# Kernel tuning notes

Hardware: AMD Instinct MI355X
Metric: run time of the kernel (lower is better)

## Reference

```python
import jax, jax.numpy as jnp
import numpy as np

N_NODES = 50000
N_EDGES = 1600000
D = 64  # in_dim = hidden_dim = out_dim
R = 8   # num_rels


def setup_inputs() -> dict:
    key = jax.random.key(0)
    ks = jax.random.split(key, 9)
    adj = jax.random.randint(ks[0], (2, N_EDGES), 0, N_NODES, dtype=jnp.int32)
    features = jax.random.normal(ks[1], (N_NODES, D), dtype=jnp.float32)
    edge_type = jax.random.randint(ks[2], (N_EDGES,), 0, R, dtype=jnp.int32)
    s = 1.0 / np.sqrt(D)
    W1 = jax.random.normal(ks[3], (R, D, D), dtype=jnp.float32) * s
    root1 = jax.random.normal(ks[4], (D, D), dtype=jnp.float32) * s
    b1 = jnp.zeros((D,), dtype=jnp.float32)
    W2 = jax.random.normal(ks[5], (R, D, D), dtype=jnp.float32) * s
    root2 = jax.random.normal(ks[6], (D, D), dtype=jnp.float32) * s
    b2 = jnp.zeros((D,), dtype=jnp.float32)
    return {"adj": adj, "features": features, "edge_type": edge_type,
            "W1": W1, "root1": root1, "b1": b1,
            "W2": W2, "root2": root2, "b2": b2}


def _rgcn_layer(x, edge_index, edge_type, W, root, bias):
    # FastRGCNConv, aggr='add': out_i = sum_{(j,r)->i} W_r x_j + root^T x_i + b
    src, dst = edge_index[0], edge_index[1]
    # pre-transform all nodes under every relation: [R, N, F]
    h = jnp.einsum('nd,rdf->rnf', x, W)
    msg = h[edge_type, src]                      # [E, F] gather per edge
    agg = jax.ops.segment_sum(msg, dst, num_segments=x.shape[0])
    return agg + x @ root + bias


def reference(adj, features, edge_type, W1, root1, b1, W2, root2, b2):
    x = _rgcn_layer(features, adj, edge_type, W1, root1, b1)
    x = jax.nn.relu(x)
    x = _rgcn_layer(x, adj, edge_type, W2, root2, b2)
    return x
```

## Files before the change

### kernel.cpp

```cpp
#include <hip/hip_runtime.h>
#include <cstdint>
#include <cstddef>

#define DF 64
#define NREL 8
#define DPB 64
#define DPB_SHIFT 6
#define NBMAX 1024
#define EPB 4096
#define BCAP 3072
#define NKEY 512

typedef __attribute__((ext_vector_type(8))) short bf16x8;
typedef __attribute__((ext_vector_type(4))) float f32x4;

static __device__ __forceinline__ unsigned short f2bf(float f) {
  unsigned int u = __float_as_uint(f);
  u += 0x7FFFu + ((u >> 16) & 1u);
  return (unsigned short)(u >> 16);
}
static __device__ __forceinline__ float bf2f(unsigned short s) {
  return __uint_as_float((unsigned int)s << 16);
}

__global__ __launch_bounds__(512) void prep(
    const float* __restrict__ W1, const float* __restrict__ rt1,
    const float* __restrict__ W2, const float* __restrict__ rt2,
    bf16x8* __restrict__ frag,
    const float* __restrict__ x, unsigned short* __restrict__ xb, int n8,
    int* __restrict__ bcnt, int NB)
{
  const int b = blockIdx.x;
  const int t = threadIdx.x;

  if (b < 18) {
    const float* W = (b < 8)  ? (W1 + (size_t)b * 4096)
                   : (b == 8) ? rt1
                   : (b < 17) ? (W2 + (size_t)(b - 9) * 4096)
                              : rt2;
    const int ft = t >> 7;
    const int ks = (t >> 6) & 1;
    const int l  = t & 63;
    const int col = ft * 16 + (l & 15);
    const int k0  = ks * 32 + (l >> 4) * 8;
    bf16x8 f;
#pragma unroll
    for (int j = 0; j < 8; ++j)
      f[j] = (short)f2bf(W[(size_t)(k0 + j) * 64 + col]);
    frag[(((size_t)b * 4 + ft) * 2 + ks) * 64 + l] = f;
    return;
  }

  if (b == 18) {
    for (int i = t; i < NB; i += 512) bcnt[i] = 0;
  }

  const int i = (b - 18) * 512 + t;
  if (i < n8) {
    const float4 v0 = *(const float4*)&x[(size_t)i * 8];
    const float4 v1 = *(const float4*)&x[(size_t)i * 8 + 4];
    uint4 pk;
    pk.x = (unsigned)f2bf(v0.x) | ((unsigned)f2bf(v0.y) << 16);
    pk.y = (unsigned)f2bf(v0.z) | ((unsigned)f2bf(v0.w) << 16);
    pk.z = (unsigned)f2bf(v1.x) | ((unsigned)f2bf(v1.y) << 16);
    pk.w = (unsigned)f2bf(v1.z) | ((unsigned)f2bf(v1.w) << 16);
    *(uint4*)&xb[(size_t)i * 8] = pk;
  }
}

__global__ __launch_bounds__(512) void bucket_count(
    const int* __restrict__ dst, int* __restrict__ bcnt,
    int* __restrict__ relof, int E, int NB)
{
  __shared__ int lh[NBMAX];
  const int t = threadIdx.x;
  for (int i = t; i < NB; i += 512) lh[i] = 0;
  __syncthreads();
  const int base = blockIdx.x * EPB;
  const int cnt = min(EPB, E - base);
  for (int k = t; k < cnt; k += 512)
    atomicAdd(&lh[dst[base + k] >> DPB_SHIFT], 1);
  __syncthreads();
  int* rrow = relof + (size_t)blockIdx.x * NB;
  for (int i = t; i < NB; i += 512) {
    int c = lh[i];
    rrow[i] = c ? atomicAdd(&bcnt[i], c) : 0;
  }
}

__global__ __launch_bounds__(1024) void scan_buckets(
    const int* __restrict__ bcnt, int* __restrict__ boff, int NB, int E)
{
  __shared__ int sc[1024];
  const int t = threadIdx.x;
  int v = (t < NB) ? bcnt[t] : 0;
  sc[t] = v;
  __syncthreads();
  for (int off = 1; off < 1024; off <<= 1) {
    int u = (t >= off) ? sc[t - off] : 0;
    __syncthreads();
    sc[t] += u;
    __syncthreads();
  }
  if (t < NB) boff[t] = sc[t] - v;
  if (t == 0) boff[NB] = E;
}

__global__ __launch_bounds__(512) void bin_scatter(
    const int* __restrict__ src, const int* __restrict__ dst,
    const int* __restrict__ et,
    const int* __restrict__ boff, const int* __restrict__ relof,
    unsigned int* __restrict__ binned, int E, int NB)
{
  __shared__ int cur[NBMAX];
  const int t = threadIdx.x;
  const int* rrow = relof + (size_t)blockIdx.x * NB;
  for (int i = t; i < NB; i += 512) cur[i] = boff[i] + rrow[i];
  __syncthreads();
  const int base = blockIdx.x * EPB;
  const int cnt = min(EPB, E - base);
  for (int k = t; k < cnt; k += 512) {
    int e = base + k;
    int d = dst[e];
    int pos = atomicAdd(&cur[d >> DPB_SHIFT], 1);
    binned[pos] = ((unsigned)et[e] << 24) | ((unsigned)src[e] << 7) |
                  ((unsigned)d & (DPB - 1));
  }
}

static __device__ __forceinline__ void gadd(
    float* __restrict__ acc, const uint4& u)
{
  acc[0] += bf2f((unsigned short)u.x);
  acc[1] += bf2f((unsigned short)(u.x >> 16));
  acc[2] += bf2f((unsigned short)u.y);
  acc[3] += bf2f((unsigned short)(u.y >> 16));
  acc[4] += bf2f((unsigned short)u.z);
  acc[5] += bf2f((unsigned short)(u.z >> 16));
  acc[6] += bf2f((unsigned short)u.w);
  acc[7] += bf2f((unsigned short)(u.w >> 16));
}

__global__ __launch_bounds__(512) void gather_sum(
    const unsigned int* __restrict__ binned,
    const int* __restrict__ boff,
    const unsigned short* __restrict__ xb,
    unsigned short* __restrict__ s,
    int N)
{
  __shared__ unsigned int srt[BCAP];
  __shared__ int h[NKEY], sc[NKEY], cur[NKEY];
  __shared__ int wsum[8];
  const int t = threadIdx.x;
  const int b = blockIdx.x;
  const int beg = boff[b], end = boff[b + 1];
  const int m = min(end - beg, BCAP);

  h[t] = 0;
  __syncthreads();
  for (int k = t; k < m; k += 512) {
    unsigned w = binned[beg + k];
    atomicAdd(&h[((w & (DPB - 1)) << 3) | (w >> 24)], 1);
  }
  __syncthreads();

  {
    const int lane = t & 63;
    const int wv = t >> 6;
    int v = h[t];
    int incl = v;
#pragma unroll
    for (int off = 1; off < 64; off <<= 1) {
      int u = __shfl_up(incl, off);
      if (lane >= off) incl += u;
    }
    if (lane == 63) wsum[wv] = incl;
    __syncthreads();
    int wo = 0;
    for (int w2 = 0; w2 < wv; ++w2) wo += wsum[w2];
    sc[t] = incl + wo;
    cur[t] = sc[t] - v;
  }
  __syncthreads();

  for (int k = t; k < m; k += 512) {
    unsigned w = binned[beg + k];
    int pos = atomicAdd(&cur[((w & (DPB - 1)) << 3) | (w >> 24)], 1);
    srt[pos] = w;
  }
  __syncthreads();

  const int nl = t >> 3;
  const int node = (b << DPB_SHIFT) + nl;
  const int l8 = (t & 7) * 8;
  if (node >= N) return;
  const int ovf = end - beg - BCAP;

#define XADDR(wv) ((const uint4*)&xb[(((size_t)(((wv) >> 7) & 0x1FFFFu)) << 6) + l8])
  for (int r = 0; r < NREL; ++r) {
    const int kk = (nl << 3) | r;
    int p = sc[kk] - h[kk];
    const int pe = sc[kk];
    float acc[8];
#pragma unroll
    for (int i = 0; i < 8; ++i) acc[i] = 0.f;

    for (; p + 3 < pe; p += 4) {
      unsigned w0 = srt[p],     w1 = srt[p + 1];
      unsigned w2 = srt[p + 2], w3 = srt[p + 3];
      uint4 u0 = *XADDR(w0), u1 = *XADDR(w1);
      uint4 u2 = *XADDR(w2), u3 = *XADDR(w3);
      gadd(acc, u0); gadd(acc, u1); gadd(acc, u2); gadd(acc, u3);
    }
    for (; p < pe; ++p) {
      unsigned w0 = srt[p];
      uint4 u0 = *XADDR(w0);
      gadd(acc, u0);
    }
    if (ovf > 0) {
      for (int k = 0; k < ovf; ++k) {
        unsigned w0 = binned[beg + BCAP + k];
        if ((int)(w0 & (DPB - 1)) == nl && (int)(w0 >> 24) == r) {
          uint4 u0 = *XADDR(w0);
          gadd(acc, u0);
        }
      }
    }

    uint4 pk;
    pk.x = (unsigned)f2bf(acc[0]) | ((unsigned)f2bf(acc[1]) << 16);
    pk.y = (unsigned)f2bf(acc[2]) | ((unsigned)f2bf(acc[3]) << 16);
    pk.z = (unsigned)f2bf(acc[4]) | ((unsigned)f2bf(acc[5]) << 16);
    pk.w = (unsigned)f2bf(acc[6]) | ((unsigned)f2bf(acc[7]) << 16);
    *(uint4*)&s[(((size_t)node * NREL + r) << 6) + l8] = pk;
  }
#undef XADDR
}

__global__ __launch_bounds__(256) void gemm_fused(
    const unsigned short* __restrict__ s,
    const unsigned short* __restrict__ xb,
    const bf16x8* __restrict__ wfrag,
    const float* __restrict__ bias,
    float* __restrict__ out,
    unsigned short* __restrict__ xbn,
    int N, int do_relu)
{
  const int tid = threadIdx.x;
  const int l  = tid & 63;
  const int w  = tid >> 6;
  const int n0 = blockIdx.x * 128 + w * 32;
  const int lr = l & 15;
  const int lg = l >> 4;

  f32x4 acc[4][2];
#pragma unroll
  for (int mt = 0; mt < 4; ++mt)
#pragma unroll
    for (int nt = 0; nt < 2; ++nt)
      acc[mt][nt] = (f32x4)(0.f);

  const int node0 = n0 + lr;
  const int node1 = n0 + 16 + lr;

  for (int r = 0; r < 9; ++r) {
    const bf16x8* wf = wfrag + (size_t)r * 512;
    bf16x8 a[4][2];
#pragma unroll
    for (int mt = 0; mt < 4; ++mt)
#pragma unroll
      for (int ks = 0; ks < 2; ++ks)
        a[mt][ks] = wf[(mt * 2 + ks) * 64 + l];

    bf16x8 b[2][2];
#pragma unroll
    for (int nt = 0; nt < 2; ++nt) {
      const int node = nt ? node1 : node0;
#pragma unroll
      for (int ks = 0; ks < 2; ++ks) {
        if (node < N) {
          const unsigned short* bp = (r < 8)
              ? &s[(((size_t)node * NREL + r) << 6) + ks * 32 + lg * 8]
              : &xb[((size_t)node << 6) + ks * 32 + lg * 8];
          b[nt][ks] = *(const bf16x8*)bp;
        } else {
          b[nt][ks] = (bf16x8)(short)0;
        }
      }
    }

#pragma unroll
    for (int ks = 0; ks < 2; ++ks)
#pragma unroll
      for (int mt = 0; mt < 4; ++mt)
#pragma unroll
        for (int nt = 0; nt < 2; ++nt)
          acc[mt][nt] = __builtin_amdgcn_mfma_f32_16x16x32_bf16(
              a[mt][ks], b[nt][ks], acc[mt][nt], 0, 0, 0);
  }

#pragma unroll
  for (int nt = 0; nt < 2; ++nt) {
    const int node = nt ? node1 : node0;
    if (node < N) {
#pragma unroll
      for (int mt = 0; mt < 4; ++mt) {
        const int f0 = mt * 16 + lg * 4;
        float4 bb = *(const float4*)&bias[f0];
        float4 v = make_float4(acc[mt][nt][0] + bb.x,
                               acc[mt][nt][1] + bb.y,
                               acc[mt][nt][2] + bb.z,
                               acc[mt][nt][3] + bb.w);
        if (do_relu) {
          v.x = fmaxf(v.x, 0.f); v.y = fmaxf(v.y, 0.f);
          v.z = fmaxf(v.z, 0.f); v.w = fmaxf(v.w, 0.f);
        }
        *(float4*)&out[((size_t)node << 6) + f0] = v;
        if (xbn) {
          uint2 pk;
          pk.x = (unsigned)f2bf(v.x) | ((unsigned)f2bf(v.y) << 16);
          pk.y = (unsigned)f2bf(v.z) | ((unsigned)f2bf(v.w) << 16);
          *(uint2*)&xbn[((size_t)node << 6) + f0] = pk;
        }
      }
    }
  }
}

__global__ __launch_bounds__(128) void rgcn_transform(
    const float* __restrict__ x,
    const float* __restrict__ Wc,
    unsigned short* __restrict__ hb,
    int N)
{
  const int r = blockIdx.y;
  const float* W = Wc + (size_t)r * DF * DF;

  __shared__ float Ws[DF * DF];
  __shared__ float Xs[128 * 65];

  const int tid = threadIdx.x;
  const int n0 = blockIdx.x * 128;
  const int nrem = N - n0;

  {
    const float4* Wv = (const float4*)W;
    float4* Wsv = (float4*)Ws;
#pragma unroll
    for (int j = 0; j < 8; ++j) Wsv[tid + j * 128] = Wv[tid + j * 128];
  }
#pragma unroll
  for (int j = 0; j < 16; ++j) {
    int idx = tid + j * 128;
    int n = idx >> 4;
    int c4 = (idx & 15) * 4;
    float4 v = make_float4(0.f, 0.f, 0.f, 0.f);
    if (n < nrem) v = *(const float4*)&x[(size_t)(n0 + n) * DF + c4];
    float* p = &Xs[n * 65 + c4];
    p[0] = v.x; p[1] = v.y; p[2] = v.z; p[3] = v.w;
  }
  __syncthreads();

  const int fg = (tid & 7) * 8;
  const int ng = (tid >> 3) * 8;

  float4 a0[8], a1[8];
#pragma unroll
  for (int i = 0; i < 8; ++i) {
    a0[i] = make_float4(0.f, 0.f, 0.f, 0.f);
    a1[i] = make_float4(0.f, 0.f, 0.f, 0.f);
  }

#pragma unroll 4
  for (int d = 0; d < DF; ++d) {
    float4 w0 = *(const float4*)&Ws[d * DF + fg];
    float4 w1 = *(const float4*)&Ws[d * DF + fg + 4];
#pragma unroll
    for (int i = 0; i < 8; ++i) {
      float xv = Xs[(ng + i) * 65 + d];
      a0[i].x += xv * w0.x; a0[i].y += xv * w0.y;
      a0[i].z += xv * w0.z; a0[i].w += xv * w0.w;
      a1[i].x += xv * w1.x; a1[i].y += xv * w1.y;
      a1[i].z += xv * w1.z; a1[i].w += xv * w1.w;
    }
  }

#pragma unroll
  for (int i = 0; i < 8; ++i) {
    int n = ng + i;
    if (n < nrem) {
      uint4 pk;
      pk.x = (unsigned)f2bf(a0[i].x) | ((unsigned)f2bf(a0[i].y) << 16);
      pk.y = (unsigned)f2bf(a0[i].z) | ((unsigned)f2bf(a0[i].w) << 16);
      pk.z = (unsigned)f2bf(a1[i].x) | ((unsigned)f2bf(a1[i].y) << 16);
      pk.w = (unsigned)f2bf(a1[i].z) | ((unsigned)f2bf(a1[i].w) << 16);
      unsigned short* op = hb + (((size_t)r * N + (n0 + n)) << 6) + fg;
      *(uint4*)op = pk;
    }
  }
}

__global__ __launch_bounds__(128) void rgcn_root_epilogue(
    const float* __restrict__ x,
    const float* __restrict__ root,
    const float* __restrict__ bias,
    float* __restrict__ out,
    int N, int mode)
{
  __shared__ float Ws[DF * DF];
  __shared__ float Xs[128 * 65];

  const int tid = threadIdx.x;
  const int n0 = blockIdx.x * 128;
  const int nrem = N - n0;

  {
    const float4* Wv = (const float4*)root;
    float4* Wsv = (float4*)Ws;
#pragma unroll
    for (int j = 0; j < 8; ++j) Wsv[tid + j * 128] = Wv[tid + j * 128];
  }
#pragma unroll
  for (int j = 0; j < 16; ++j) {
    int idx = tid + j * 128;
    int n = idx >> 4;
    int c4 = (idx & 15) * 4;
    float4 v = make_float4(0.f, 0.f, 0.f, 0.f);
    if (n < nrem) v = *(const float4*)&x[(size_t)(n0 + n) * DF + c4];
    float* p = &Xs[n * 65 + c4];
    p[0] = v.x; p[1] = v.y; p[2] = v.z; p[3] = v.w;
  }
  __syncthreads();

  const int fg = (tid & 7) * 8;
  const int ng = (tid >> 3) * 8;

  float4 a0[8], a1[8];
#pragma unroll
  for (int i = 0; i < 8; ++i) {
    a0[i] = make_float4(0.f, 0.f, 0.f, 0.f);
    a1[i] = make_float4(0.f, 0.f, 0.f, 0.f);
  }

#pragma unroll 4
  for (int d = 0; d < DF; ++d) {
    float4 w0 = *(const float4*)&Ws[d * DF + fg];
    float4 w1 = *(const float4*)&Ws[d * DF + fg + 4];
#pragma unroll
    for (int i = 0; i < 8; ++i) {
      float xv = Xs[(ng + i) * 65 + d];
      a0[i].x += xv * w0.x; a0[i].y += xv * w0.y;
      a0[i].z += xv * w0.z; a0[i].w += xv * w0.w;
      a1[i].x += xv * w1.x; a1[i].y += xv * w1.y;
      a1[i].z += xv * w1.z; a1[i].w += xv * w1.w;
    }
  }

  float4 bb0 = *(const float4*)&bias[fg];
  float4 bb1 = *(const float4*)&bias[fg + 4];

#pragma unroll
  for (int i = 0; i < 8; ++i) {
    int n = ng + i;
    if (n < nrem) {
      float* op = out + (size_t)(n0 + n) * DF + fg;
      float4 o0 = *(float4*)op;
      float4 o1 = *(float4*)(op + 4);
      o0.x += a0[i].x + bb0.x; o0.y += a0[i].y + bb0.y;
      o0.z += a0[i].z + bb0.z; o0.w += a0[i].w + bb0.w;
      o1.x += a1[i].x + bb1.x; o1.y += a1[i].y + bb1.y;
      o1.z += a1[i].z + bb1.z; o1.w += a1[i].w + bb1.w;
      if (mode == 1) {
        o0.x = fmaxf(o0.x, 0.f); o0.y = fmaxf(o0.y, 0.f);
        o0.z = fmaxf(o0.z, 0.f); o0.w = fmaxf(o0.w, 0.f);
        o1.x = fmaxf(o1.x, 0.f); o1.y = fmaxf(o1.y, 0.f);
        o1.z = fmaxf(o1.z, 0.f); o1.w = fmaxf(o1.w, 0.f);
      }
      *(float4*)op = o0;
      *(float4*)(op + 4) = o1;
    }
  }
}

__global__ __launch_bounds__(256) void rgcn_scatter(
    const int* __restrict__ src, const int* __restrict__ dst,
    const int* __restrict__ et,
    const unsigned short* __restrict__ hb,
    float* __restrict__ out,
    int E, int N, int r0, int r1)
{
  long long g = (long long)blockIdx.x * 256 + threadIdx.x;
  int e = (int)(g >> 4);
  if (e >= E) return;
  int r = et[e];
  if (r < r0 || r >= r1) return;
  int f4 = ((int)g & 15) * 4;
  int s = src[e];
  int d = dst[e];
  ushort4 u = *(const ushort4*)&hb[(((size_t)(r - r0) * N + s) << 6) + f4];
  float* o = out + ((size_t)d << 6) + f4;
  atomicAdd(o + 0, bf2f(u.x));
  atomicAdd(o + 1, bf2f(u.y));
  atomicAdd(o + 2, bf2f(u.z));
  atomicAdd(o + 3, bf2f(u.w));
}

extern "C" void kernel_launch(void* const* d_in, const int* in_sizes, int n_in,
                              void* d_out, int out_size, void* d_ws, size_t ws_size,
                              hipStream_t stream) {
  const int* adj    = (const int*)d_in[0];
  const float* feat = (const float*)d_in[1];
  const int* et     = (const int*)d_in[2];
  const float* W1   = (const float*)d_in[3];
  const float* rt1  = (const float*)d_in[4];
  const float* b1   = (const float*)d_in[5];
  const float* W2   = (const float*)d_in[6];
  const float* rt2  = (const float*)d_in[7];
  const float* b2   = (const float*)d_in[8];

  const int E = in_sizes[0] / 2;
  const int N = in_sizes[1] / DF;
  const int* srcp = adj;
  const int* dstp = adj + E;

  float* out = (float*)d_out;
  const size_t ND = (size_t)N * DF;
  const int nblk = (N + 127) / 128;
  const int NB = (N + DPB - 1) >> DPB_SHIFT;
  const int ebk = (E + EPB - 1) / EPB;

  const size_t wfrag_elems = (size_t)18 * 512;
  const size_t need = 8 * ND * 2 + ND * 2 + ND * 2 + wfrag_elems * 16 +
                      (size_t)E * 4 + (size_t)ebk * NB * 4 +
                      ((size_t)2 * NB + 1) * 4;

  if (ws_size >= need && NB <= NBMAX && N < (1 << 17)) {
    unsigned short* s   = (unsigned short*)d_ws;
    unsigned short* xb  = s + 8 * ND;
    unsigned short* xb2 = xb + ND;
    bf16x8* wfrag = (bf16x8*)(xb2 + ND);
    unsigned int* binned = (unsigned int*)(wfrag + wfrag_elems);
    int* relof = (int*)(binned + E);
    int* bcnt = relof + (size_t)ebk * NB;
    int* boff = bcnt + NB;

    const int n8 = (int)(ND / 8);
    prep<<<18 + (n8 + 511) / 512, 512, 0, stream>>>(
        W1, rt1, W2, rt2, wfrag, feat, xb, n8, bcnt, NB);

    bucket_count<<<ebk, 512, 0, stream>>>(dstp, bcnt, relof, E, NB);
    scan_buckets<<<1, 1024, 0, stream>>>(bcnt, boff, NB, E);
    bin_scatter<<<ebk, 512, 0, stream>>>(srcp, dstp, et, boff, relof,
                                         binned, E, NB);

    gather_sum<<<NB, 512, 0, stream>>>(binned, boff, xb, s, N);
    gemm_fused<<<nblk, 256, 0, stream>>>(s, xb, wfrag, b1, out, xb2, N, 1);

    gather_sum<<<NB, 512, 0, stream>>>(binned, boff, xb2, s, N);
    gemm_fused<<<nblk, 256, 0, stream>>>(s, xb2, wfrag + (size_t)9 * 512,
                                         b2, out, nullptr, N, 0);
    return;
  }

  size_t per_rel = ND * sizeof(unsigned short);
  size_t xmid_b = ND * sizeof(float);
  int RC = 1;
  if (ws_size > per_rel + xmid_b) {
    size_t rc = (ws_size - xmid_b) / per_rel;
    RC = rc >= NREL ? NREL : (int)rc;
  }
  unsigned short* hb = (unsigned short*)d_ws;
  float* xmid = (float*)((char*)d_ws + (size_t)RC * per_rel);
  const int sblk = (int)(((size_t)E * 16 + 255) / 256);

  for (int layer = 0; layer < 2; ++layer) {
    const float* xin = layer ? xmid : feat;
    const float* W   = layer ? W2 : W1;
    const float* rt  = layer ? rt2 : rt1;
    const float* bs  = layer ? b2 : b1;
    float* o         = layer ? out : xmid;

    hipMemsetAsync(o, 0, ND * sizeof(float), stream);
    for (int r0 = 0; r0 < NREL; r0 += RC) {
      int rc = (NREL - r0) < RC ? (NREL - r0) : RC;
      rgcn_transform<<<dim3(nblk, rc), 128, 0, stream>>>(
          xin, W + (size_t)r0 * DF * DF, hb, N);
      rgcn_scatter<<<sblk, 256, 0, stream>>>(
          srcp, dstp, et, hb, o, E, N, r0, r0 + rc);
    }
    rgcn_root_epilogue<<<nblk, 128, 0, stream>>>(xin, rt, bs, o, N,
                                                 layer == 0 ? 1 : 2);
  }
}
```

Measured before the change: 150.2 us.

## Fuse per-relation gather-sum with MFMA transform into one kernel per layer

```diff
diff --git a/kernel.cpp b/kernel.cpp
--- a/kernel.cpp
+++ b/kernel.cpp
@@ -10,6 +10,7 @@
 #define EPB 4096
 #define BCAP 3072
 #define NKEY 512
+#define SBST 72
 
 typedef __attribute__((ext_vector_type(8))) short bf16x8;
 typedef __attribute__((ext_vector_type(4))) float f32x4;
@@ -141,104 +142,9 @@
   acc[7] += bf2f((unsigned short)(u.w >> 16));
 }
 
-__global__ __launch_bounds__(512) void gather_sum(
+__global__ __launch_bounds__(512, 4) void gather_gemm(
     const unsigned int* __restrict__ binned,
     const int* __restrict__ boff,
-    const unsigned short* __restrict__ xb,
-    unsigned short* __restrict__ s,
-    int N)
-{
-  __shared__ unsigned int srt[BCAP];
-  __shared__ int h[NKEY], sc[NKEY], cur[NKEY];
-  __shared__ int wsum[8];
-  const int t = threadIdx.x;
-  const int b = blockIdx.x;
-  const int beg = boff[b], end = boff[b + 1];
-  const int m = min(end - beg, BCAP);
-
-  h[t] = 0;
-  __syncthreads();
-  for (int k = t; k < m; k += 512) {
-    unsigned w = binned[beg + k];
-    atomicAdd(&h[((w & (DPB - 1)) << 3) | (w >> 24)], 1);
-  }
-  __syncthreads();
-
-  {
-    const int lane = t & 63;
-    const int wv = t >> 6;
-    int v = h[t];
-    int incl = v;
-#pragma unroll
-    for (int off = 1; off < 64; off <<= 1) {
-      int u = __shfl_up(incl, off);
-      if (lane >= off) incl += u;
-    }
-    if (lane == 63) wsum[wv] = incl;
-    __syncthreads();
-    int wo = 0;
-    for (int w2 = 0; w2 < wv; ++w2) wo += wsum[w2];
-    sc[t] = incl + wo;
-    cur[t] = sc[t] - v;
-  }
-  __syncthreads();
-
-  for (int k = t; k < m; k += 512) {
-    unsigned w = binned[beg + k];
-    int pos = atomicAdd(&cur[((w & (DPB - 1)) << 3) | (w >> 24)], 1);
-    srt[pos] = w;
-  }
-  __syncthreads();
-
-  const int nl = t >> 3;
-  const int node = (b << DPB_SHIFT) + nl;
-  const int l8 = (t & 7) * 8;
-  if (node >= N) return;
-  const int ovf = end - beg - BCAP;
-
-#define XADDR(wv) ((const uint4*)&xb[(((size_t)(((wv) >> 7) & 0x1FFFFu)) << 6) + l8])
-  for (int r = 0; r < NREL; ++r) {
-    const int kk = (nl << 3) | r;
-    int p = sc[kk] - h[kk];
-    const int pe = sc[kk];
-    float acc[8];
-#pragma unroll
-    for (int i = 0; i < 8; ++i) acc[i] = 0.f;
-
-    for (; p + 3 < pe; p += 4) {
-      unsigned w0 = srt[p],     w1 = srt[p + 1];
-      unsigned w2 = srt[p + 2], w3 = srt[p + 3];
-      uint4 u0 = *XADDR(w0), u1 = *XADDR(w1);
-      uint4 u2 = *XADDR(w2), u3 = *XADDR(w3);
-      gadd(acc, u0); gadd(acc, u1); gadd(acc, u2); gadd(acc, u3);
-    }
-    for (; p < pe; ++p) {
-      unsigned w0 = srt[p];
-      uint4 u0 = *XADDR(w0);
-      gadd(acc, u0);
-    }
-    if (ovf > 0) {
-      for (int k = 0; k < ovf; ++k) {
-        unsigned w0 = binned[beg + BCAP + k];
-        if ((int)(w0 & (DPB - 1)) == nl && (int)(w0 >> 24) == r) {
-          uint4 u0 = *XADDR(w0);
-          gadd(acc, u0);
-        }
-      }
-    }
-
-    uint4 pk;
-    pk.x = (unsigned)f2bf(acc[0]) | ((unsigned)f2bf(acc[1]) << 16);
-    pk.y = (unsigned)f2bf(acc[2]) | ((unsigned)f2bf(acc[3]) << 16);
-    pk.z = (unsigned)f2bf(acc[4]) | ((unsigned)f2bf(acc[5]) << 16);
-    pk.w = (unsigned)f2bf(acc[6]) | ((unsigned)f2bf(acc[7]) << 16);
-    *(uint4*)&s[(((size_t)node * NREL + r) << 6) + l8] = pk;
-  }
-#undef XADDR
-}
-
-__global__ __launch_bounds__(256) void gemm_fused(
-    const unsigned short* __restrict__ s,
     const unsigned short* __restrict__ xb,
     const bf16x8* __restrict__ wfrag,
     const float* __restrict__ bias,
@@ -246,82 +152,164 @@
     unsigned short* __restrict__ xbn,
     int N, int do_relu)
 {
-  const int tid = threadIdx.x;
-  const int l  = tid & 63;
-  const int w  = tid >> 6;
-  const int n0 = blockIdx.x * 128 + w * 32;
-  const int lr = l & 15;
-  const int lg = l >> 4;
-
-  f32x4 acc[4][2];
-#pragma unroll
-  for (int mt = 0; mt < 4; ++mt)
-#pragma unroll
-    for (int nt = 0; nt < 2; ++nt)
-      acc[mt][nt] = (f32x4)(0.f);
-
-  const int node0 = n0 + lr;
-  const int node1 = n0 + 16 + lr;
-
-  for (int r = 0; r < 9; ++r) {
-    const bf16x8* wf = wfrag + (size_t)r * 512;
-    bf16x8 a[4][2];
-#pragma unroll
-    for (int mt = 0; mt < 4; ++mt)
-#pragma unroll
-      for (int ks = 0; ks < 2; ++ks)
-        a[mt][ks] = wf[(mt * 2 + ks) * 64 + l];
-
-    bf16x8 b[2][2];
-#pragma unroll
-    for (int nt = 0; nt < 2; ++nt) {
-      const int node = nt ? node1 : node0;
-#pragma unroll
-      for (int ks = 0; ks < 2; ++ks) {
-        if (node < N) {
-          const unsigned short* bp = (r < 8)
-              ? &s[(((size_t)node * NREL + r) << 6) + ks * 32 + lg * 8]
-              : &xb[((size_t)node << 6) + ks * 32 + lg * 8];
-          b[nt][ks] = *(const bf16x8*)bp;
-        } else {
-          b[nt][ks] = (bf16x8)(short)0;
+  __shared__ unsigned int srt[BCAP];
+  __shared__ int h[NKEY], sc[NKEY], cur[NKEY];
+  __shared__ int wsum[8];
+  __shared__ unsigned short sbuf[64 * SBST];
+
+  const int t = threadIdx.x;
+  const int b = blockIdx.x;
+  const int beg = boff[b], end = boff[b + 1];
+  const int m = min(end - beg, BCAP);
+
+  h[t] = 0;
+  __syncthreads();
+  for (int k = t; k < m; k += 512) {
+    unsigned w = binned[beg + k];
+    atomicAdd(&h[((w & (DPB - 1)) << 3) | (w >> 24)], 1);
+  }
+  __syncthreads();
+  {
+    const int lane = t & 63;
+    const int wvv = t >> 6;
+    int v = h[t];
+    int incl = v;
+#pragma unroll
+    for (int off = 1; off < 64; off <<= 1) {
+      int u = __shfl_up(incl, off);
+      if (lane >= off) incl += u;
+    }
+    if (lane == 63) wsum[wvv] = incl;
+    __syncthreads();
+    int wo = 0;
+    for (int w2 = 0; w2 < wvv; ++w2) wo += wsum[w2];
+    sc[t] = incl + wo;
+    cur[t] = sc[t] - v;
+  }
+  __syncthreads();
+  for (int k = t; k < m; k += 512) {
+    unsigned w = binned[beg + k];
+    int pos = atomicAdd(&cur[((w & (DPB - 1)) << 3) | (w >> 24)], 1);
+    srt[pos] = w;
+  }
+  __syncthreads();
+
+  const int nl = t >> 3;
+  const int l8 = (t & 7) * 8;
+  const int ovf = end - beg - BCAP;
+
+  float acc[NREL][8];
+#pragma unroll
+  for (int r = 0; r < NREL; ++r)
+#pragma unroll
+    for (int i = 0; i < 8; ++i) acc[r][i] = 0.f;
+
+#define XADDR(wv) ((const uint4*)&xb[(((size_t)(((wv) >> 7) & 0x1FFFFu)) << 6) + l8])
+#pragma unroll
+  for (int r = 0; r < NREL; ++r) {
+    const int kk = (nl << 3) | r;
+    int p = sc[kk] - h[kk];
+    const int pe = sc[kk];
+    for (; p + 3 < pe; p += 4) {
+      unsigned w0 = srt[p],     w1 = srt[p + 1];
+      unsigned w2 = srt[p + 2], w3 = srt[p + 3];
+      uint4 u0 = *XADDR(w0), u1 = *XADDR(w1);
+      uint4 u2 = *XADDR(w2), u3 = *XADDR(w3);
+      gadd(acc[r], u0); gadd(acc[r], u1); gadd(acc[r], u2); gadd(acc[r], u3);
+    }
+    for (; p < pe; ++p) {
+      unsigned w0 = srt[p];
+      uint4 u0 = *XADDR(w0);
+      gadd(acc[r], u0);
+    }
+    if (ovf > 0) {
+      for (int k = 0; k < ovf; ++k) {
+        unsigned w0 = binned[beg + BCAP + k];
+        if ((int)(w0 & (DPB - 1)) == nl && (int)(w0 >> 24) == r) {
+          uint4 u0 = *XADDR(w0);
+          gadd(acc[r], u0);
         }
       }
     }
-
+  }
+#undef XADDR
+
+  const int l   = t & 63;
+  const int wv  = t >> 6;
+  const int lr  = l & 15;
+  const int lg  = l >> 4;
+  const int ng  = wv & 3;
+  const int mtb = (wv >> 2) * 2;
+
+  f32x4 accm[2];
+  accm[0] = (f32x4)(0.f);
+  accm[1] = (f32x4)(0.f);
+
+#pragma unroll
+  for (int r = 0; r < NREL; ++r) {
+    uint4 pk;
+    pk.x = (unsigned)f2bf(acc[r][0]) | ((unsigned)f2bf(acc[r][1]) << 16);
+    pk.y = (unsigned)f2bf(acc[r][2]) | ((unsigned)f2bf(acc[r][3]) << 16);
+    pk.z = (unsigned)f2bf(acc[r][4]) | ((unsigned)f2bf(acc[r][5]) << 16);
+    pk.w = (unsigned)f2bf(acc[r][6]) | ((unsigned)f2bf(acc[r][7]) << 16);
+    *(uint4*)&sbuf[nl * SBST + l8] = pk;
+    __syncthreads();
+
+    bf16x8 bfr[2];
 #pragma unroll
     for (int ks = 0; ks < 2; ++ks)
-#pragma unroll
-      for (int mt = 0; mt < 4; ++mt)
-#pragma unroll
-        for (int nt = 0; nt < 2; ++nt)
-          acc[mt][nt] = __builtin_amdgcn_mfma_f32_16x16x32_bf16(
-              a[mt][ks], b[nt][ks], acc[mt][nt], 0, 0, 0);
-  }
-
-#pragma unroll
-  for (int nt = 0; nt < 2; ++nt) {
-    const int node = nt ? node1 : node0;
-    if (node < N) {
-#pragma unroll
-      for (int mt = 0; mt < 4; ++mt) {
-        const int f0 = mt * 16 + lg * 4;
-        float4 bb = *(const float4*)&bias[f0];
-        float4 v = make_float4(acc[mt][nt][0] + bb.x,
-                               acc[mt][nt][1] + bb.y,
-                               acc[mt][nt][2] + bb.z,
-                               acc[mt][nt][3] + bb.w);
-        if (do_relu) {
-          v.x = fmaxf(v.x, 0.f); v.y = fmaxf(v.y, 0.f);
-          v.z = fmaxf(v.z, 0.f); v.w = fmaxf(v.w, 0.f);
-        }
-        *(float4*)&out[((size_t)node << 6) + f0] = v;
-        if (xbn) {
-          uint2 pk;
-          pk.x = (unsigned)f2bf(v.x) | ((unsigned)f2bf(v.y) << 16);
-          pk.y = (unsigned)f2bf(v.z) | ((unsigned)f2bf(v.w) << 16);
-          *(uint2*)&xbn[((size_t)node << 6) + f0] = pk;
-        }
+      bfr[ks] = *(const bf16x8*)&sbuf[(ng * 16 + lr) * SBST + ks * 32 + lg * 8];
+
+    const bf16x8* wf = wfrag + (size_t)r * 512;
+#pragma unroll
+    for (int i = 0; i < 2; ++i)
+#pragma unroll
+      for (int ks = 0; ks < 2; ++ks) {
+        bf16x8 a = wf[((mtb + i) * 2 + ks) * 64 + l];
+        accm[i] = __builtin_amdgcn_mfma_f32_16x16x32_bf16(a, bfr[ks], accm[i],
+                                                          0, 0, 0);
+      }
+    __syncthreads();
+  }
+
+  const int node = (b << DPB_SHIFT) + ng * 16 + lr;
+  {
+    bf16x8 bfr[2];
+#pragma unroll
+    for (int ks = 0; ks < 2; ++ks) {
+      if (node < N)
+        bfr[ks] = *(const bf16x8*)&xb[((size_t)node << 6) + ks * 32 + lg * 8];
+      else
+        bfr[ks] = (bf16x8)(short)0;
+    }
+    const bf16x8* wf = wfrag + (size_t)8 * 512;
+#pragma unroll
+    for (int i = 0; i < 2; ++i)
+#pragma unroll
+      for (int ks = 0; ks < 2; ++ks) {
+        bf16x8 a = wf[((mtb + i) * 2 + ks) * 64 + l];
+        accm[i] = __builtin_amdgcn_mfma_f32_16x16x32_bf16(a, bfr[ks], accm[i],
+                                                          0, 0, 0);
+      }
+  }
+
+  if (node < N) {
+#pragma unroll
+    for (int i = 0; i < 2; ++i) {
+      const int f0 = (mtb + i) * 16 + lg * 4;
+      float4 bb = *(const float4*)&bias[f0];
+      float4 v = make_float4(accm[i][0] + bb.x, accm[i][1] + bb.y,
+                             accm[i][2] + bb.z, accm[i][3] + bb.w);
+      if (do_relu) {
+        v.x = fmaxf(v.x, 0.f); v.y = fmaxf(v.y, 0.f);
+        v.z = fmaxf(v.z, 0.f); v.w = fmaxf(v.w, 0.f);
+      }
+      *(float4*)&out[((size_t)node << 6) + f0] = v;
+      if (xbn) {
+        uint2 pk;
+        pk.x = (unsigned)f2bf(v.x) | ((unsigned)f2bf(v.y) << 16);
+        pk.y = (unsigned)f2bf(v.z) | ((unsigned)f2bf(v.w) << 16);
+        *(uint2*)&xbn[((size_t)node << 6) + f0] = pk;
       }
     }
   }
@@ -525,18 +513,16 @@
 
   float* out = (float*)d_out;
   const size_t ND = (size_t)N * DF;
-  const int nblk = (N + 127) / 128;
   const int NB = (N + DPB - 1) >> DPB_SHIFT;
   const int ebk = (E + EPB - 1) / EPB;
 
   const size_t wfrag_elems = (size_t)18 * 512;
-  const size_t need = 8 * ND * 2 + ND * 2 + ND * 2 + wfrag_elems * 16 +
+  const size_t need = ND * 2 + ND * 2 + wfrag_elems * 16 +
                       (size_t)E * 4 + (size_t)ebk * NB * 4 +
                       ((size_t)2 * NB + 1) * 4;
 
   if (ws_size >= need && NB <= NBMAX && N < (1 << 17)) {
-    unsigned short* s   = (unsigned short*)d_ws;
-    unsigned short* xb  = s + 8 * ND;
+    unsigned short* xb  = (unsigned short*)d_ws;
     unsigned short* xb2 = xb + ND;
     bf16x8* wfrag = (bf16x8*)(xb2 + ND);
     unsigned int* binned = (unsigned int*)(wfrag + wfrag_elems);
@@ -553,15 +539,15 @@
     bin_scatter<<<ebk, 512, 0, stream>>>(srcp, dstp, et, boff, relof,
                                          binned, E, NB);
 
-    gather_sum<<<NB, 512, 0, stream>>>(binned, boff, xb, s, N);
-    gemm_fused<<<nblk, 256, 0, stream>>>(s, xb, wfrag, b1, out, xb2, N, 1);
-
-    gather_sum<<<NB, 512, 0, stream>>>(binned, boff, xb2, s, N);
-    gemm_fused<<<nblk, 256, 0, stream>>>(s, xb2, wfrag + (size_t)9 * 512,
-                                         b2, out, nullptr, N, 0);
+    gather_gemm<<<NB, 512, 0, stream>>>(binned, boff, xb, wfrag, b1,
+                                        out, xb2, N, 1);
+    gather_gemm<<<NB, 512, 0, stream>>>(binned, boff, xb2,
+                                        wfrag + (size_t)9 * 512, b2,
+                                        out, nullptr, N, 0);
     return;
   }
 
+  const int nblk = (N + 127) / 128;
   size_t per_rel = ND * sizeof(unsigned short);
   size_t xmid_b = ND * sizeof(float);
   int RC = 1;
```

Measured after the change: 157.3 us. 4.7% more time.
